# Performance work log

Hardware: AMD Instinct MI355X
Metric: run time of the kernel (lower is better)

The kernel has to match this reference:

```python
import jax, jax.numpy as jnp
import numpy as np

N_CLUSTERS = 256
EMBED_DIM = 128
ALPHA = 1.0


def setup_inputs() -> dict:
    key = jax.random.key(0)
    k1, k2 = jax.random.split(key)
    inputs = jax.random.normal(k1, (200000, EMBED_DIM), dtype=jnp.float32)
    clusters = jax.random.normal(k2, (N_CLUSTERS, EMBED_DIM), dtype=jnp.float32)
    return {"inputs": inputs, "clusters": clusters}


def reference(inputs, clusters):
    # Squared euclidean distance via the GEMM trick instead of an [N, K, D]
    x_sq = jnp.sum(inputs * inputs, axis=1, keepdims=True)          # [N, 1]
    c_sq = jnp.sum(clusters * clusters, axis=1)[None, :]             # [1, K]
    cross = inputs @ clusters.T                                      # [N, K]
    dist2 = jnp.maximum(x_sq + c_sq - 2.0 * cross, 0.0)              # [N, K]
    q = 1.0 / (1.0 + dist2 / ALPHA)
    q = q ** ((ALPHA + 1.0) / 2.0)
    q = q / jnp.sum(q, axis=1, keepdims=True)
    return q
```

## Files before the change

kernel.cpp:

```cpp
#include <hip/hip_runtime.h>


#define DIM 128
#define NK  256

typedef __attribute__((ext_vector_type(8))) short short8;
typedef __attribute__((ext_vector_type(4))) float floatx4;

__device__ __forceinline__ unsigned short bf16_rne(float f) {
    unsigned int u = __float_as_uint(f);
    return (unsigned short)((u + 0x7fffu + ((u >> 16) & 1u)) >> 16);
}
__device__ __forceinline__ float bf16_f(unsigned short h) {
    return __uint_as_float(((unsigned int)h) << 16);
}

__global__ void prep_clusters(const float* __restrict__ c,
                              unsigned short* __restrict__ wb,
                              float* __restrict__ wcsq)
{
    if (blockIdx.x < 8) {
        const int gid  = blockIdx.x * 512 + threadIdx.x;
        const int lane = gid & 63;
        const int ks   = (gid >> 6) & 3;
        const int ct   = gid >> 8;
        const int lm   = lane & 15;
        const int q4   = lane >> 4;
        const int col  = ct * 16 + lm;
        const float4* cg = (const float4*)(c + col * DIM + ks * 32 + q4 * 8);
        float4 v0 = cg[0], v1 = cg[1];
        const float* f0 = (const float*)&v0;
        const float* f1 = (const float*)&v1;
        union { unsigned short u[8]; short8 v; } B;
        #pragma unroll
        for (int i = 0; i < 4; ++i) B.u[i] = bf16_rne(f0[i]);
        #pragma unroll
        for (int i = 0; i < 4; ++i) B.u[4 + i] = bf16_rne(f1[i]);
        ((short8*)wb)[gid] = B.v;
    } else {
        const int t = threadIdx.x;
        const int col = t >> 1, half = t & 1;
        const float4* cg = (const float4*)(c + col * DIM + half * 64);
        float s = 0.f;
        #pragma unroll
        for (int i = 0; i < 16; ++i) {
            float4 v = cg[i];
            s = fmaf(v.x, v.x, s); s = fmaf(v.y, v.y, s);
            s = fmaf(v.z, v.z, s); s = fmaf(v.w, v.w, s);
        }
        s += __shfl_xor(s, 1);
        if (!half) wcsq[col] = s;
    }
}

__global__ __launch_bounds__(256, 3) void cluster_q_v4(
    const float* __restrict__ x,
    const unsigned short* __restrict__ wb,
    const float* __restrict__ wcsq,
    float* __restrict__ out)
{
    __shared__ float csq_s[NK];
    __shared__ __align__(16) float lt[4][2][4][264];

    const int tid  = threadIdx.x;
    csq_s[tid] = wcsq[tid];

    const int wave = tid >> 6;
    const int lane = tid & 63;
    const int lm   = lane & 15;
    const int q4   = lane >> 4;
    const size_t row0 = (size_t)blockIdx.x * 64 + wave * 16;

    short8 ah[4], al[4];
    float xq = 0.f;
    const float* xrow = x + (row0 + lm) * DIM;
    #pragma unroll
    for (int ks = 0; ks < 4; ++ks) {
        const float4* xg = (const float4*)(xrow + ks * 32 + q4 * 8);
        float4 v0 = xg[0], v1 = xg[1];
        const float* f0 = (const float*)&v0;
        const float* f1 = (const float*)&v1;
        union { unsigned short u[8]; short8 v; } H, L;
        #pragma unroll
        for (int i = 0; i < 4; ++i) {
            float f = f0[i];
            xq = fmaf(f, f, xq);
            unsigned short h = bf16_rne(f);
            H.u[i] = h;
            L.u[i] = bf16_rne(f - bf16_f(h));
        }
        #pragma unroll
        for (int i = 0; i < 4; ++i) {
            float f = f1[i];
            xq = fmaf(f, f, xq);
            unsigned short h = bf16_rne(f);
            H.u[4 + i] = h;
            L.u[4 + i] = bf16_rne(f - bf16_f(h));
        }
        ah[ks] = H.v;
        al[ks] = L.v;
    }
    xq += __shfl_xor(xq, 16);
    xq += __shfl_xor(xq, 32);

    floatx4 acc[16];
    #pragma unroll
    for (int ct = 0; ct < 16; ++ct) {
        const short8* bp = (const short8*)wb + (ct * 256 + lane);
        floatx4 a = (floatx4){0.f, 0.f, 0.f, 0.f};
        #pragma unroll
        for (int ks = 0; ks < 4; ++ks) {
            short8 b = bp[ks * 64];
            a = __builtin_amdgcn_mfma_f32_16x16x32_bf16(ah[ks], b, a, 0, 0, 0);
            a = __builtin_amdgcn_mfma_f32_16x16x32_bf16(al[ks], b, a, 0, 0, 0);
        }
        acc[ct] = a;
    }

    __syncthreads();

    float xs4[4];
    #pragma unroll
    for (int r = 0; r < 4; ++r) xs4[r] = __shfl(xq, q4 * 4 + r);

    float rsum[4] = {0.f, 0.f, 0.f, 0.f};
    #pragma unroll
    for (int ct = 0; ct < 16; ++ct) {
        const float cq = csq_s[ct * 16 + lm];
        #pragma unroll
        for (int r = 0; r < 4; ++r) {
            float d2 = fmaf(-2.f, acc[ct][r], xs4[r] + cq);
            d2 = fmaxf(d2, 0.f);
            float q = __builtin_amdgcn_rcpf(1.f + d2);
            acc[ct][r] = q;
            rsum[r] += q;
        }
    }
    #pragma unroll
    for (int r = 0; r < 4; ++r) {
        rsum[r] += __shfl_xor(rsum[r], 1);
        rsum[r] += __shfl_xor(rsum[r], 2);
        rsum[r] += __shfl_xor(rsum[r], 4);
        rsum[r] += __shfl_xor(rsum[r], 8);
        rsum[r] = __builtin_amdgcn_rcpf(rsum[r]);
    }

    #pragma unroll
    for (int r = 0; r < 4; ++r) {
        float* lw = &lt[wave][r & 1][q4][0];
        const float inv = rsum[r];
        #pragma unroll
        for (int ct = 0; ct < 16; ++ct)
            lw[ct * 16 + lm] = acc[ct][r] * inv;
        asm volatile("s_waitcnt lgkmcnt(0)" ::: "memory");
        #pragma unroll
        for (int j = 0; j < 4; ++j) {
            const floatx4 v = *(const floatx4*)&lt[wave][r & 1][j][lane * 4];
            __builtin_nontemporal_store(v, (floatx4*)(out + (row0 + j * 4 + r) * NK + lane * 4));
        }
    }
}

extern "C" void kernel_launch(void* const* d_in, const int* in_sizes, int n_in,
                              void* d_out, int out_size, void* d_ws, size_t ws_size,
                              hipStream_t stream) {
    const float* x = (const float*)d_in[0];
    const float* c = (const float*)d_in[1];
    float* out = (float*)d_out;
    unsigned short* wb = (unsigned short*)d_ws;
    float* wcsq = (float*)((char*)d_ws + 65536);
    const int N = in_sizes[0] / DIM;

    prep_clusters<<<dim3(9), dim3(512), 0, stream>>>(c, wb, wcsq);
    cluster_q_v4<<<dim3(N / 64), dim3(256), 0, stream>>>(x, wb, wcsq, out);
}
```

Before: 333.9 us.

## Make cluster kernel persistent with LDS-resident cluster weights and prefetched input tiles

Turns the one-block-per-tile kernel into a persistent kernel with at most 512 blocks looping over 64-row tiles. The bf16 cluster matrix (64 KB) is staged into shared memory once per block instead of re-read from global/L2 for each tile. The next tile's input rows are prefetched into registers while the current tile's epilogue runs. In exchange, the 64 KB of LDS and the launch bound of 1 limit occupancy to roughly one block per CU, so latency hiding rests on the manual prefetch.

```diff
diff --git a/kernel.cpp b/kernel.cpp
--- a/kernel.cpp
+++ b/kernel.cpp
@@ -53,111 +53,137 @@
     }
 }
 
-__global__ __launch_bounds__(256, 3) void cluster_q_v4(
+__device__ __forceinline__ void prefetch_x(const float* __restrict__ x,
+                                           int t, int wave, int lm, int q4,
+                                           float4 pf[8]) {
+    const float* xr = x + ((size_t)t * 64 + wave * 16 + lm) * DIM;
+    #pragma unroll
+    for (int ks = 0; ks < 4; ++ks) {
+        const float4* xg = (const float4*)(xr + ks * 32 + q4 * 8);
+        pf[2 * ks]     = xg[0];
+        pf[2 * ks + 1] = xg[1];
+    }
+}
+
+__global__ __launch_bounds__(256, 1) void cluster_q_v5(
     const float* __restrict__ x,
     const unsigned short* __restrict__ wb,
     const float* __restrict__ wcsq,
-    float* __restrict__ out)
+    float* __restrict__ out,
+    const int NT)
 {
+    __shared__ __align__(16) unsigned short bs[32768];
     __shared__ float csq_s[NK];
     __shared__ __align__(16) float lt[4][2][4][264];
 
     const int tid  = threadIdx.x;
-    csq_s[tid] = wcsq[tid];
-
     const int wave = tid >> 6;
     const int lane = tid & 63;
     const int lm   = lane & 15;
     const int q4   = lane >> 4;
-    const size_t row0 = (size_t)blockIdx.x * 64 + wave * 16;
-
-    short8 ah[4], al[4];
-    float xq = 0.f;
-    const float* xrow = x + (row0 + lm) * DIM;
-    #pragma unroll
-    for (int ks = 0; ks < 4; ++ks) {
-        const float4* xg = (const float4*)(xrow + ks * 32 + q4 * 8);
-        float4 v0 = xg[0], v1 = xg[1];
-        const float* f0 = (const float*)&v0;
-        const float* f1 = (const float*)&v1;
-        union { unsigned short u[8]; short8 v; } H, L;
-        #pragma unroll
-        for (int i = 0; i < 4; ++i) {
-            float f = f0[i];
-            xq = fmaf(f, f, xq);
-            unsigned short h = bf16_rne(f);
-            H.u[i] = h;
-            L.u[i] = bf16_rne(f - bf16_f(h));
-        }
-        #pragma unroll
-        for (int i = 0; i < 4; ++i) {
-            float f = f1[i];
-            xq = fmaf(f, f, xq);
-            unsigned short h = bf16_rne(f);
-            H.u[4 + i] = h;
-            L.u[4 + i] = bf16_rne(f - bf16_f(h));
-        }
-        ah[ks] = H.v;
-        al[ks] = L.v;
-    }
-    xq += __shfl_xor(xq, 16);
-    xq += __shfl_xor(xq, 32);
-
-    floatx4 acc[16];
-    #pragma unroll
-    for (int ct = 0; ct < 16; ++ct) {
-        const short8* bp = (const short8*)wb + (ct * 256 + lane);
-        floatx4 a = (floatx4){0.f, 0.f, 0.f, 0.f};
+
+    csq_s[tid] = wcsq[tid];
+    for (int i = tid; i < 4096; i += 256) {
+        float4 v = ((const float4*)wb)[i];
+        *(float4*)&bs[i * 8] = v;
+    }
+    __syncthreads();
+
+    float4 pf[8];
+    int t = blockIdx.x;
+    if (t < NT) prefetch_x(x, t, wave, lm, q4, pf);
+
+    while (t < NT) {
+        short8 ah[4], al[4];
+        float xq = 0.f;
         #pragma unroll
         for (int ks = 0; ks < 4; ++ks) {
-            short8 b = bp[ks * 64];
-            a = __builtin_amdgcn_mfma_f32_16x16x32_bf16(ah[ks], b, a, 0, 0, 0);
-            a = __builtin_amdgcn_mfma_f32_16x16x32_bf16(al[ks], b, a, 0, 0, 0);
-        }
-        acc[ct] = a;
-    }
-
-    __syncthreads();
-
-    float xs4[4];
-    #pragma unroll
-    for (int r = 0; r < 4; ++r) xs4[r] = __shfl(xq, q4 * 4 + r);
-
-    float rsum[4] = {0.f, 0.f, 0.f, 0.f};
-    #pragma unroll
-    for (int ct = 0; ct < 16; ++ct) {
-        const float cq = csq_s[ct * 16 + lm];
+            const float* f0 = (const float*)&pf[2 * ks];
+            const float* f1 = (const float*)&pf[2 * ks + 1];
+            union { unsigned short u[8]; short8 v; } H, L;
+            #pragma unroll
+            for (int i = 0; i < 4; ++i) {
+                float f = f0[i];
+                xq = fmaf(f, f, xq);
+                unsigned short h = bf16_rne(f);
+                H.u[i] = h;
+                L.u[i] = bf16_rne(f - bf16_f(h));
+            }
+            #pragma unroll
+            for (int i = 0; i < 4; ++i) {
+                float f = f1[i];
+                xq = fmaf(f, f, xq);
+                unsigned short h = bf16_rne(f);
+                H.u[4 + i] = h;
+                L.u[4 + i] = bf16_rne(f - bf16_f(h));
+            }
+            ah[ks] = H.v;
+            al[ks] = L.v;
+        }
+        xq += __shfl_xor(xq, 16);
+        xq += __shfl_xor(xq, 32);
+
+        floatx4 acc[16];
+        #pragma unroll
+        for (int ct = 0; ct < 16; ++ct) {
+            floatx4 a = (floatx4){0.f, 0.f, 0.f, 0.f};
+            #pragma unroll
+            for (int ks = 0; ks < 4; ++ks) {
+                short8 b = *(const short8*)&bs[(ct * 256 + ks * 64 + lane) * 8];
+                a = __builtin_amdgcn_mfma_f32_16x16x32_bf16(ah[ks], b, a, 0, 0, 0);
+                a = __builtin_amdgcn_mfma_f32_16x16x32_bf16(al[ks], b, a, 0, 0, 0);
+            }
+            acc[ct] = a;
+        }
+
+        const int tn = t + (int)gridDim.x;
+        if (tn < NT) prefetch_x(x, tn, wave, lm, q4, pf);
+
+        float xs4[4];
+        #pragma unroll
+        for (int r = 0; r < 4; ++r) xs4[r] = __shfl(xq, q4 * 4 + r);
+
+        float rsum[4] = {0.f, 0.f, 0.f, 0.f};
+        #pragma unroll
+        for (int ct = 0; ct < 16; ++ct) {
+            const float cq = csq_s[ct * 16 + lm];
+            #pragma unroll
+            for (int r = 0; r < 4; ++r) {
+                float d2 = fmaf(-2.f, acc[ct][r], xs4[r] + cq);
+                d2 = fmaxf(d2, 0.f);
+                float q = __builtin_amdgcn_rcpf(1.f + d2);
+                acc[ct][r] = q;
+                rsum[r] += q;
+            }
+        }
         #pragma unroll
         for (int r = 0; r < 4; ++r) {
-            float d2 = fmaf(-2.f, acc[ct][r], xs4[r] + cq);
-            d2 = fmaxf(d2, 0.f);
-            float q = __builtin_amdgcn_rcpf(1.f + d2);
-            acc[ct][r] = q;
-            rsum[r] += q;
-        }
-    }
-    #pragma unroll
-    for (int r = 0; r < 4; ++r) {
-        rsum[r] += __shfl_xor(rsum[r], 1);
-        rsum[r] += __shfl_xor(rsum[r], 2);
-        rsum[r] += __shfl_xor(rsum[r], 4);
-        rsum[r] += __shfl_xor(rsum[r], 8);
-        rsum[r] = __builtin_amdgcn_rcpf(rsum[r]);
-    }
-
-    #pragma unroll
-    for (int r = 0; r < 4; ++r) {
-        float* lw = &lt[wave][r & 1][q4][0];
-        const float inv = rsum[r];
-        #pragma unroll
-        for (int ct = 0; ct < 16; ++ct)
-            lw[ct * 16 + lm] = acc[ct][r] * inv;
-        asm volatile("s_waitcnt lgkmcnt(0)" ::: "memory");
-        #pragma unroll
-        for (int j = 0; j < 4; ++j) {
-            const floatx4 v = *(const floatx4*)&lt[wave][r & 1][j][lane * 4];
-            __builtin_nontemporal_store(v, (floatx4*)(out + (row0 + j * 4 + r) * NK + lane * 4));
-        }
+            rsum[r] += __shfl_xor(rsum[r], 1);
+            rsum[r] += __shfl_xor(rsum[r], 2);
+            rsum[r] += __shfl_xor(rsum[r], 4);
+            rsum[r] += __shfl_xor(rsum[r], 8);
+            rsum[r] = __builtin_amdgcn_rcpf(rsum[r]);
+        }
+
+        __builtin_amdgcn_sched_barrier(0);
+
+        #pragma unroll
+        for (int r = 0; r < 4; ++r) {
+            float* lw = &lt[wave][r & 1][q4][0];
+            const float inv = rsum[r];
+            #pragma unroll
+            for (int ct = 0; ct < 16; ++ct)
+                lw[ct * 16 + lm] = acc[ct][r] * inv;
+            asm volatile("s_waitcnt lgkmcnt(0)" ::: "memory");
+            #pragma unroll
+            for (int j = 0; j < 4; ++j) {
+                const floatx4 v = *(const floatx4*)&lt[wave][r & 1][j][lane * 4];
+                __builtin_nontemporal_store(v,
+                    (floatx4*)(out + ((size_t)t * 64 + wave * 16 + j * 4 + r) * NK + lane * 4));
+            }
+        }
+
+        t = tn;
     }
 }
 
@@ -170,7 +196,9 @@
     unsigned short* wb = (unsigned short*)d_ws;
     float* wcsq = (float*)((char*)d_ws + 65536);
     const int N = in_sizes[0] / DIM;
+    const int NT = N / 64;
 
     prep_clusters<<<dim3(9), dim3(512), 0, stream>>>(c, wb, wcsq);
-    cluster_q_v4<<<dim3(N / 64), dim3(256), 0, stream>>>(x, wb, wcsq, out);
-}
+    const int grid = NT < 512 ? NT : 512;
+    cluster_q_v5<<<dim3(grid), dim3(256), 0, stream>>>(x, wb, wcsq, out, NT);
+}
```

Result: faster. 289.9 us (-13.2%).
